# Optimization experiments

Measured on AMD Instinct MI355X. Metric: run time of the kernel, lower is better.

## Reference

```python
import jax, jax.numpy as jnp
import numpy as np

D = 1024; H = 8; QLR = 384; KVLR = 256; NOPE = 128; ROPE = 64; VD = 128
E = 8; TOPK = 2; INTER = 512; NSH = 2; B = 2; T = 2048
QKD = NOPE + ROPE  # 192


def _rms(x, w, eps=1e-6):
    return x * jax.lax.rsqrt(jnp.mean(x * x, axis=-1, keepdims=True) + eps) * w


def _rope(x, cos, sin):
    # x: [B,T,h,ROPE]; pairs are consecutive elements (torch view(...,-1,2)).
    x0 = x[..., 0::2]
    x1 = x[..., 1::2]
    c = cos[None, :, None, :]
    s = sin[None, :, None, :]
    y0 = x0 * c - x1 * s
    y1 = x0 * s + x1 * c
    return jnp.stack([y0, y1], axis=-1).reshape(x.shape)


def setup_inputs() -> dict:
    key = jax.random.key(0)
    ks = jax.random.split(key, 12)
    def w(k, shape, scale=0.02):
        return jax.random.normal(k, shape, dtype=jnp.float32) * scale
    inv = 1.0 / (10000.0 ** (jnp.arange(0, ROPE, 2, dtype=jnp.float32) / ROPE))
    ang = jnp.arange(T, dtype=jnp.float32)[:, None] * inv[None, :]  # [T, ROPE//2]
    return {
        "x": jax.random.normal(ks[0], (B, T, D), dtype=jnp.float32),
        "freqs_cos": jnp.cos(ang),
        "freqs_sin": jnp.sin(ang),
        "rmsn1_w": jnp.ones((D,), jnp.float32),
        "rmsn2_w": jnp.ones((D,), jnp.float32),
        "latent_w": w(ks[1], (D, QLR + KVLR + ROPE)),
        "q_norm_w": jnp.ones((QLR,), jnp.float32),
        "q_up_w": w(ks[2], (QLR, H * QKD)),
        "kv_norm_w": jnp.ones((KVLR,), jnp.float32),
        "kv_up_w": w(ks[3], (KVLR, H * (NOPE + VD))),
        "c_proj_w": w(ks[4], (D, D)),
        "gate_w": w(ks[5], (D, E)),
        "sh_w1": w(ks[6], (D, INTER * NSH)),
        "sh_w2": w(ks[7], (INTER * NSH, D)),
        "sh_w3": w(ks[8], (D, INTER * NSH)),
        "e_w1": w(ks[9], (E, D, INTER)),
        "e_w2": w(ks[10], (E, INTER, D)),
        "e_w3": w(ks[11], (E, D, INTER)),
    }


def reference(x, freqs_cos, freqs_sin, rmsn1_w, rmsn2_w, latent_w, q_norm_w,
              q_up_w, kv_norm_w, kv_up_w, c_proj_w, gate_w, sh_w1, sh_w2,
              sh_w3, e_w1, e_w2, e_w3):
    Bx, Tx, _ = x.shape
    # ---- MLA attention ----
    h = _rms(x, rmsn1_w)
    lat = h @ latent_w
    q_l, kv_l, k_r = jnp.split(lat, [QLR, QLR + KVLR], axis=-1)
    q = (_rms(q_l, q_norm_w) @ q_up_w).reshape(Bx, Tx, H, QKD)
    q_n, q_r = q[..., :NOPE], q[..., NOPE:]
    q_r = _rope(q_r, freqs_cos, freqs_sin)
    q = jnp.concatenate([q_n, q_r], axis=-1)  # [B,T,H,QKD]
    kv = (_rms(kv_l, kv_norm_w) @ kv_up_w).reshape(Bx, Tx, H, NOPE + VD)
    k_n, v = kv[..., :NOPE], kv[..., NOPE:]
    k_r = _rope(k_r[:, :, None, :], freqs_cos, freqs_sin)
    k_r = jnp.broadcast_to(k_r, (Bx, Tx, H, ROPE))
    k = jnp.concatenate([k_n, k_r], axis=-1)
    scale = 1.0 / jnp.sqrt(jnp.float32(QKD))
    scores = jnp.einsum('bqhd,bkhd->bhqk', q, k) * scale
    causal = jnp.tril(jnp.ones((Tx, Tx), dtype=bool))
    scores = jnp.where(causal, scores, jnp.finfo(scores.dtype).min)
    attn = jax.nn.softmax(scores, axis=-1)
    y = jnp.einsum('bhqk,bkhd->bqhd', attn, v).reshape(Bx, Tx, D)
    x = x + y @ c_proj_w
    # ---- DeepSeekMoE ----
    h2 = _rms(x, rmsn2_w).reshape(-1, D)  # [N, D]
    y_sh = (jax.nn.silu(h2 @ sh_w1) * (h2 @ sh_w3)) @ sh_w2
    scores_g = jax.nn.softmax(h2 @ gate_w, axis=-1)  # [N, E]
    w_top, idx = jax.lax.top_k(scores_g, TOPK)  # weights == gathered original scores
    # combine weights per expert (route_scale = 1.0)
    cw = jnp.sum(jax.nn.one_hot(idx, E, dtype=h2.dtype) * w_top[..., None], axis=1)  # [N, E]
    h1 = jnp.einsum('nd,edi->eni', h2, e_w1)
    h3 = jnp.einsum('nd,edi->eni', h2, e_w3)
    out_e = jnp.einsum('eni,eid->end', jax.nn.silu(h1) * h3, e_w2)  # [E, N, D]
    y_moe = y_sh + jnp.einsum('end,ne->nd', out_e, cw)
    return x + y_moe.reshape(Bx, Tx, D)
```

## Files before the change

### kernel.cpp

```cpp
#include <hip/hip_runtime.h>
#include <hip/hip_bf16.h>
#include <math.h>

#define D_ 1024
#define H_ 8
#define QLR_ 384
#define KVLR_ 256
#define NOPE_ 128
#define ROPE_ 64
#define VD_ 128
#define E_ 8
#define INTER_ 512
#define B_ 2
#define T_ 2048
#define QKD_ 192
#define NTOK (B_*T_)
#define LSTR 4608
#define MAXMB 72

typedef __attribute__((ext_vector_type(8))) short short8;
typedef __attribute__((ext_vector_type(4))) float f32x4;
typedef __attribute__((ext_vector_type(4))) unsigned short us4;

__device__ __forceinline__ unsigned short f2bf(float f) {
  union { float f; unsigned u; } v; v.f = f;
  return (unsigned short)((v.u + 0x7FFFu + ((v.u >> 16) & 1u)) >> 16);
}
__device__ __forceinline__ float bf2f(unsigned short h) {
  union { unsigned u; float f; } v; v.u = ((unsigned)h) << 16;
  return v.f;
}

#define GLD16(SRC, DST) __builtin_amdgcn_global_load_lds( \
    (__attribute__((address_space(1))) void*)(SRC), \
    (__attribute__((address_space(3))) void*)(DST), 16, 0, 0)

#define DPPF(v, ctrl) __int_as_float(__builtin_amdgcn_update_dpp(0, __float_as_int(v), ctrl, 0xF, 0xF, true))
__device__ __forceinline__ float dppmax16(float v) {
  v = fmaxf(v, DPPF(v, 0xB1));
  v = fmaxf(v, DPPF(v, 0x4E));
  v = fmaxf(v, DPPF(v, 0x124));
  v = fmaxf(v, DPPF(v, 0x128));
  return v;
}
__device__ __forceinline__ float dppsum16(float v) {
  v += DPPF(v, 0xB1);
  v += DPPF(v, 0x4E);
  v += DPPF(v, 0x124);
  v += DPPF(v, 0x128);
  return v;
}

__global__ __launch_bounds__(256) void transpose_f32_bf16(
    const float* __restrict__ in, unsigned short* __restrict__ out,
    int R, int C, size_t inBS, size_t outBS) {
  __shared__ float tile[32][33];
  const float* inp = in + (size_t)blockIdx.z * inBS;
  unsigned short* outp = out + (size_t)blockIdx.z * outBS;
  int c0 = blockIdx.x * 32, r0 = blockIdx.y * 32;
  int tx = threadIdx.x & 31, ty = threadIdx.x >> 5;
  #pragma unroll
  for (int i = 0; i < 4; ++i) {
    int rr = ty + i * 8;
    tile[rr][tx] = inp[(size_t)(r0 + rr) * C + c0 + tx];
  }
  __syncthreads();
  #pragma unroll
  for (int i = 0; i < 4; ++i) {
    int rr = ty + i * 8;
    outp[(size_t)(c0 + rr) * R + r0 + tx] = f2bf(tile[tx][rr]);
  }
}

__global__ __launch_bounds__(256) void transpose_pair(
    const float* __restrict__ in1, const float* __restrict__ in3,
    unsigned short* __restrict__ out, int K, int C1, size_t inBS, size_t outBS) {
  __shared__ float tile[32][33];
  int z = blockIdx.z; int bat = z >> 1; int f = (z & 1) * 16;
  const float* src = ((z & 1) ? in3 : in1) + (size_t)bat * inBS;
  unsigned short* o = out + (size_t)bat * outBS;
  int c0 = blockIdx.x * 32, r0 = blockIdx.y * 32;
  int tx = threadIdx.x & 31, ty = threadIdx.x >> 5;
  #pragma unroll
  for (int i = 0; i < 4; ++i) {
    int rr = ty + i * 8;
    tile[rr][tx] = src[(size_t)(r0 + rr) * C1 + c0 + tx];
  }
  __syncthreads();
  #pragma unroll
  for (int i = 0; i < 4; ++i) {
    int cc = ty + i * 8;
    int c = c0 + cc;
    int n = ((c >> 4) << 5) + (c & 15) + f;
    o[(size_t)n * K + r0 + tx] = f2bf(tile[tx][cc]);
  }
}

template<typename TI>
__global__ __launch_bounds__(256) void rms_to_bf16(
    const TI* __restrict__ src, int stride, int off, const float* __restrict__ w,
    unsigned short* __restrict__ out, int Dd, int outStride) {
  int row = blockIdx.x;
  const TI* xr = src + (size_t)row * stride + off;
  float ss = 0.f;
  for (int i = threadIdx.x; i < Dd; i += 256) {
    float v;
    if constexpr (sizeof(TI) == 2) v = bf2f((unsigned short)xr[i]); else v = (float)xr[i];
    ss += v * v;
  }
  for (int o = 1; o < 64; o <<= 1) ss += __shfl_xor(ss, o);
  __shared__ float red[4];
  if ((threadIdx.x & 63) == 0) red[threadIdx.x >> 6] = ss;
  __syncthreads();
  float tot = red[0] + red[1] + red[2] + red[3];
  float inv = 1.f / sqrtf(tot / Dd + 1e-6f);
  for (int i = threadIdx.x; i < Dd; i += 256) {
    float v;
    if constexpr (sizeof(TI) == 2) v = bf2f((unsigned short)xr[i]); else v = (float)xr[i];
    out[(size_t)row * outStride + i] = f2bf(v * inv * w[i]);
  }
}

__global__ __launch_bounds__(256) void lat_post(
    const unsigned short* __restrict__ lat, const float* __restrict__ qw,
    const float* __restrict__ kw, const float* __restrict__ fc, const float* __restrict__ fs,
    unsigned short* __restrict__ qn, unsigned short* __restrict__ kvn,
    unsigned short* __restrict__ kr) {
  int row = blockIdx.x, tid = threadIdx.x;
  int lane = tid & 63, wv = tid >> 6;
  const unsigned short* lr = lat + (size_t)row * 768;
  float s1 = 0.f, s2 = 0.f;
  for (int i = tid; i < QLR_; i += 256) { float v = bf2f(lr[i]); s1 += v * v; }
  { float v = bf2f(lr[QLR_ + tid]); s2 = v * v; }
  for (int o = 1; o < 64; o <<= 1) { s1 += __shfl_xor(s1, o); s2 += __shfl_xor(s2, o); }
  __shared__ float red[8];
  if (lane == 0) { red[wv] = s1; red[4 + wv] = s2; }
  __syncthreads();
  float inv1 = 1.f / sqrtf((red[0] + red[1] + red[2] + red[3]) / QLR_ + 1e-6f);
  float inv2 = 1.f / sqrtf((red[4] + red[5] + red[6] + red[7]) / KVLR_ + 1e-6f);
  for (int i = tid; i < QLR_; i += 256)
    qn[(size_t)row * QLR_ + i] = f2bf(bf2f(lr[i]) * inv1 * qw[i]);
  kvn[(size_t)row * KVLR_ + tid] = f2bf(bf2f(lr[QLR_ + tid]) * inv2 * kw[tid]);
  if (tid < 32) {
    int t = row & (T_ - 1);
    float c = fc[t * 32 + tid], s = fs[t * 32 + tid];
    float x0 = bf2f(lr[640 + 2 * tid]), x1 = bf2f(lr[640 + 2 * tid + 1]);
    kr[(size_t)row * ROPE_ + 2 * tid]     = f2bf(x0 * c - x1 * s);
    kr[(size_t)row * ROPE_ + 2 * tid + 1] = f2bf(x0 * s + x1 * c);
  }
}

template<int MODE>
__global__ __launch_bounds__(256) void gemm_bf16(
    const unsigned short* __restrict__ A, const unsigned short* __restrict__ Bt,
    void* __restrict__ Cv, int M, int N, int K,
    const float* __restrict__ addv, unsigned short* __restrict__ vtg) {
  __shared__ __align__(16) unsigned short As[128 * 32];
  __shared__ __align__(16) unsigned short Bs[128 * 32];
  const int tid = threadIdx.x;
  const int lane = tid & 63, wave = tid >> 6;
  const int wm = wave >> 1, wn = wave & 1;
  const int bm = blockIdx.y * 128, bn = blockIdx.x * 128;
  const int r = lane & 15, g = lane >> 4;

  f32x4 acc[4][4];
  #pragma unroll
  for (int i = 0; i < 4; ++i)
    #pragma unroll
    for (int j = 0; j < 4; ++j) acc[i][j] = (f32x4)0.f;

  const int rl0 = wave * 16 + (lane >> 2);
  const int rl1 = rl0 + 64;
  const int kc = (lane & 3) * 8;
  char* AsB = (char*)As; char* BsB = (char*)Bs;

  for (int k0 = 0; k0 < K; k0 += 32) {
    GLD16(A + (size_t)(bm + rl0) * K + k0 + kc, AsB + wave * 1024);
    GLD16(A + (size_t)(bm + rl1) * K + k0 + kc, AsB + (wave + 4) * 1024);
    GLD16(Bt + (size_t)(bn + rl0) * K + k0 + kc, BsB + wave * 1024);
    GLD16(Bt + (size_t)(bn + rl1) * K + k0 + kc, BsB + (wave + 4) * 1024);
    __syncthreads();
    short8 af[4], bfr[4];
    #pragma unroll
    for (int mi = 0; mi < 4; ++mi)
      af[mi] = *(const short8*)(As + (wm * 64 + mi * 16 + r) * 32 + g * 8);
    #pragma unroll
    for (int nj = 0; nj < 4; ++nj)
      bfr[nj] = *(const short8*)(Bs + (wn * 64 + nj * 16 + r) * 32 + g * 8);
    #pragma unroll
    for (int mi = 0; mi < 4; ++mi)
      #pragma unroll
      for (int nj = 0; nj < 4; ++nj)
        acc[mi][nj] = __builtin_amdgcn_mfma_f32_16x16x32_bf16(af[mi], bfr[nj], acc[mi][nj], 0, 0, 0);
    __syncthreads();
  }

  if (MODE == 5) {
    unsigned short* C = (unsigned short*)Cv;
    const int colbase = bn + wn * 64;
    const int b = bm >> 11;
    const int hh = colbase >> 8;
    if ((colbase & 255) < 128) {
      #pragma unroll
      for (int mi = 0; mi < 4; ++mi)
        #pragma unroll
        for (int reg = 0; reg < 4; ++reg) {
          int mrow = bm + wm * 64 + mi * 16 + g * 4 + reg;
          size_t bas = (size_t)mrow * N + colbase + r;
          #pragma unroll
          for (int nj = 0; nj < 4; ++nj) C[bas + nj * 16] = f2bf(acc[mi][nj][reg]);
        }
    } else {
      const int tl0 = (bm & 2047) + wm * 64 + g * 4;
      const int d0 = (colbase & 255) - 128 + r;
      const size_t bhbase = (size_t)(b * 8 + hh) * 64;
      #pragma unroll
      for (int mi = 0; mi < 4; ++mi) {
        int t = tl0 + mi * 16;
        size_t tb = (bhbase + (t >> 5)) * 4096 + (t & 31);
        #pragma unroll
        for (int nj = 0; nj < 4; ++nj) {
          int d = d0 + nj * 16;
          us4 pk;
          #pragma unroll
          for (int reg = 0; reg < 4; ++reg) pk[reg] = f2bf(acc[mi][nj][reg]);
          *(us4*)(vtg + tb + (size_t)d * 32) = pk;
        }
      }
    }
    return;
  }

  const int orow0 = wm * 64 + g * 4;
  const int ocol0 = bn + wn * 64 + r;
  #pragma unroll
  for (int mi = 0; mi < 4; ++mi) {
    #pragma unroll
    for (int reg = 0; reg < 4; ++reg) {
      int mrow = bm + orow0 + mi * 16 + reg;
      if (MODE == 4) {
        unsigned short* C = (unsigned short*)Cv;
        size_t bas2 = (size_t)mrow * (N >> 1) + ((bn + wn * 64) >> 1) + r;
        #pragma unroll
        for (int p = 0; p < 2; ++p) {
          float a = acc[mi][2 * p][reg], b3 = acc[mi][2 * p + 1][reg];
          C[bas2 + p * 16] = f2bf((a / (1.f + __expf(-a))) * b3);
        }
      } else {
        size_t bas = (size_t)mrow * N + ocol0;
        if (MODE == 0) {
          unsigned short* C = (unsigned short*)Cv;
          #pragma unroll
          for (int nj = 0; nj < 4; ++nj) C[bas + nj * 16] = f2bf(acc[mi][nj][reg]);
        } else if (MODE == 1) {
          float* C = (float*)Cv;
          #pragma unroll
          for (int nj = 0; nj < 4; ++nj) C[bas + nj * 16] = acc[mi][nj][reg] + addv[bas + nj * 16];
        } else {
          float* C = (float*)Cv;
          #pragma unroll
          for (int nj = 0; nj < 4; ++nj) C[bas + nj * 16] += acc[mi][nj][reg];
        }
      }
    }
  }
}

__global__ __launch_bounds__(256) void gemm_moe13(
    const unsigned short* __restrict__ A, const unsigned short* __restrict__ W,
    unsigned short* __restrict__ Cb,
    const int* __restrict__ lists, const int* __restrict__ map, const int* __restrict__ sbase) {
  int mb = map[blockIdx.y];
  if (mb < 0) return;
  const int e = mb >> 16, ib = mb & 0xFFFF;
  __shared__ __align__(16) unsigned short As[128 * 32];
  __shared__ __align__(16) unsigned short Bs[128 * 32];
  const int tid = threadIdx.x, lane = tid & 63, wave = tid >> 6;
  const int wm = wave >> 1, wn = wave & 1;
  const int bn = blockIdx.x * 128;
  const int r = lane & 15, g = lane >> 4;

  f32x4 acc[4][4];
  #pragma unroll
  for (int i = 0; i < 4; ++i)
    #pragma unroll
    for (int j = 0; j < 4; ++j) acc[i][j] = (f32x4)0.f;

  const int rl0 = wave * 16 + (lane >> 2), rl1 = rl0 + 64;
  const int kc = (lane & 3) * 8;
  int t0 = lists[e * LSTR + ib * 128 + rl0]; if (t0 < 0) t0 = 0;
  int t1 = lists[e * LSTR + ib * 128 + rl1]; if (t1 < 0) t1 = 0;
  const unsigned short* Wb = W + (size_t)e * 1024 * 1024;
  char* AsB = (char*)As; char* BsB = (char*)Bs;

  for (int k0 = 0; k0 < 1024; k0 += 32) {
    GLD16(A + (size_t)t0 * 1024 + k0 + kc, AsB + wave * 1024);
    GLD16(A + (size_t)t1 * 1024 + k0 + kc, AsB + (wave + 4) * 1024);
    GLD16(Wb + (size_t)(bn + rl0) * 1024 + k0 + kc, BsB + wave * 1024);
    GLD16(Wb + (size_t)(bn + rl1) * 1024 + k0 + kc, BsB + (wave + 4) * 1024);
    __syncthreads();
    short8 af[4], bfr[4];
    #pragma unroll
    for (int mi = 0; mi < 4; ++mi)
      af[mi] = *(const short8*)(As + (wm * 64 + mi * 16 + r) * 32 + g * 8);
    #pragma unroll
    for (int nj = 0; nj < 4; ++nj)
      bfr[nj] = *(const short8*)(Bs + (wn * 64 + nj * 16 + r) * 32 + g * 8);
    #pragma unroll
    for (int mi = 0; mi < 4; ++mi)
      #pragma unroll
      for (int nj = 0; nj < 4; ++nj)
        acc[mi][nj] = __builtin_amdgcn_mfma_f32_16x16x32_bf16(af[mi], bfr[nj], acc[mi][nj], 0, 0, 0);
    __syncthreads();
  }
  const int sb = sbase[e] + ib * 128;
  const int hc = ((bn + wn * 64) >> 1) + r;
  #pragma unroll
  for (int mi = 0; mi < 4; ++mi)
    #pragma unroll
    for (int reg = 0; reg < 4; ++reg) {
      int srow = sb + wm * 64 + mi * 16 + g * 4 + reg;
      #pragma unroll
      for (int p = 0; p < 2; ++p) {
        float a = acc[mi][2 * p][reg], b3 = acc[mi][2 * p + 1][reg];
        Cb[(size_t)srow * 512 + hc + p * 16] = f2bf((a / (1.f + __expf(-a))) * b3);
      }
    }
}

__global__ __launch_bounds__(256) void gemm_moe2(
    const unsigned short* __restrict__ Am, const unsigned short* __restrict__ W,
    float* __restrict__ out,
    const int* __restrict__ lists, const int* __restrict__ map, const int* __restrict__ sbase,
    const float* __restrict__ cw) {
  int mb = map[blockIdx.y];
  if (mb < 0) return;
  const int e = mb >> 16, ib = mb & 0xFFFF;
  __shared__ __align__(16) unsigned short As[128 * 32];
  __shared__ __align__(16) unsigned short Bs[128 * 32];
  const int tid = threadIdx.x, lane = tid & 63, wave = tid >> 6;
  const int wm = wave >> 1, wn = wave & 1;
  const int bn = blockIdx.x * 128;
  const int r = lane & 15, g = lane >> 4;

  f32x4 acc[4][4];
  #pragma unroll
  for (int i = 0; i < 4; ++i)
    #pragma unroll
    for (int j = 0; j < 4; ++j) acc[i][j] = (f32x4)0.f;

  const int rl0 = wave * 16 + (lane >> 2), rl1 = rl0 + 64;
  const int kc = (lane & 3) * 8;
  const int sb = sbase[e] + ib * 128;
  const unsigned short* Wb = W + (size_t)e * 512 * 1024;
  char* AsB = (char*)As; char* BsB = (char*)Bs;

  for (int k0 = 0; k0 < 512; k0 += 32) {
    GLD16(Am + (size_t)(sb + rl0) * 512 + k0 + kc, AsB + wave * 1024);
    GLD16(Am + (size_t)(sb + rl1) * 512 + k0 + kc, AsB + (wave + 4) * 1024);
    GLD16(Wb + (size_t)(bn + rl0) * 512 + k0 + kc, BsB + wave * 1024);
    GLD16(Wb + (size_t)(bn + rl1) * 512 + k0 + kc, BsB + (wave + 4) * 1024);
    __syncthreads();
    short8 af[4], bfr[4];
    #pragma unroll
    for (int mi = 0; mi < 4; ++mi)
      af[mi] = *(const short8*)(As + (wm * 64 + mi * 16 + r) * 32 + g * 8);
    #pragma unroll
    for (int nj = 0; nj < 4; ++nj)
      bfr[nj] = *(const short8*)(Bs + (wn * 64 + nj * 16 + r) * 32 + g * 8);
    #pragma unroll
    for (int mi = 0; mi < 4; ++mi)
      #pragma unroll
      for (int nj = 0; nj < 4; ++nj)
        acc[mi][nj] = __builtin_amdgcn_mfma_f32_16x16x32_bf16(af[mi], bfr[nj], acc[mi][nj], 0, 0, 0);
    __syncthreads();
  }
  const int ocol0 = bn + wn * 64 + r;
  #pragma unroll
  for (int mi = 0; mi < 4; ++mi)
    #pragma unroll
    for (int reg = 0; reg < 4; ++reg) {
      int orow = wm * 64 + mi * 16 + g * 4 + reg;
      int tok = lists[e * LSTR + ib * 128 + orow];
      if (tok >= 0) {
        float wt = cw[(size_t)tok * E_ + e];
        #pragma unroll
        for (int nj = 0; nj < 4; ++nj)
          atomicAdd(out + (size_t)tok * 1024 + ocol0 + nj * 16, acc[mi][nj][reg] * wt);
      }
    }
}

#define AQ 64
#define AK 32
#define VP 40
__global__ __launch_bounds__(256) void attn_mfma(
    const unsigned short* __restrict__ q,
    const unsigned short* __restrict__ kv,
    const unsigned short* __restrict__ kr,
    const unsigned short* __restrict__ vt,
    const float* __restrict__ fcos, const float* __restrict__ fsin,
    unsigned short* __restrict__ po,
    float* __restrict__ pml) {
  __shared__ __align__(16) unsigned short Ks[AK * 192];
  __shared__ __align__(16) unsigned short Vl[128 * VP];
  __shared__ __align__(16) unsigned short Ps[4 * 16 * VP];
  const int tid = threadIdx.x, lane = tid & 63, wave = tid >> 6;
  const int r = lane & 15, g = lane >> 4;
  const int bh = blockIdx.y, b = bh >> 3, h = bh & 7;
  const int qt = gridDim.x - 1 - blockIdx.x;
  const int q0 = qt * AQ;
  const int half = blockIdx.z;
  const int hnt = qt + 1;
  const int kb = half * hnt, ke = kb + hnt;
  const size_t bT = (size_t)b * T_;
  const unsigned short* vbase = vt + (size_t)bh * 64 * 4096;
  char* KsB = (char*)Ks;

  short8 qf[6];
  const int qrow = q0 + wave * 16 + r;
  {
    const unsigned short* qb = q + ((bT + qrow) * H_ + h) * 192;
    #pragma unroll
    for (int kk = 0; kk < 6; ++kk) qf[kk] = *(const short8*)(qb + kk * 32 + g * 8);
    #pragma unroll
    for (int kk = 4; kk < 6; ++kk) {
      int i0 = (kk - 4) * 16 + g * 4;
      #pragma unroll
      for (int p = 0; p < 4; ++p) {
        float cc = fcos[qrow * 32 + i0 + p], sn = fsin[qrow * 32 + i0 + p];
        float x0 = bf2f((unsigned short)qf[kk][2 * p]), x1 = bf2f((unsigned short)qf[kk][2 * p + 1]);
        qf[kk][2 * p]     = (short)f2bf(x0 * cc - x1 * sn);
        qf[kk][2 * p + 1] = (short)f2bf(x0 * sn + x1 * cc);
      }
    }
  }

  float m_i[4], l_i[4];
  f32x4 o[8];
  #pragma unroll
  for (int i = 0; i < 4; ++i) { m_i[i] = -1e30f; l_i[i] = 0.f; }
  #pragma unroll
  for (int cb = 0; cb < 8; ++cb) o[cb] = (f32x4)0.f;

  const float scale2 = 0.07216878364870322f * 1.44269504088896f;

  short8 kreg[3], vreg[2];
  int krow[3], kcol[3];
  #pragma unroll
  for (int it = 0; it < 3; ++it) {
    int c = tid + it * 256;
    krow[it] = c / 24; kcol[it] = c % 24;
    kreg[it] = (kcol[it] < 16)
      ? *(const short8*)(kv + ((bT + kb * AK + krow[it]) * H_ + h) * 256 + kcol[it] * 8)
      : *(const short8*)(kr + (bT + kb * AK + krow[it]) * 64 + (kcol[it] - 16) * 8);
  }
  #pragma unroll
  for (int it = 0; it < 2; ++it) {
    int x = tid + it * 256;
    vreg[it] = *(const short8*)(vbase + (size_t)kb * 4096 + x * 8);
  }

  for (int kt = kb; kt < ke; ++kt) {
    __builtin_amdgcn_s_barrier();
    __builtin_amdgcn_sched_barrier(0);
    #pragma unroll
    for (int it = 0; it < 3; ++it)
      *(short8*)(KsB + ((krow[it] * 384 + kcol[it] * 16) ^ ((krow[it] & 7) << 4))) = kreg[it];
    #pragma unroll
    for (int it = 0; it < 2; ++it) {
      int x = tid + it * 256;
      *(short8*)(Vl + (x >> 2) * VP + (x & 3) * 8) = vreg[it];
    }
    asm volatile("s_waitcnt lgkmcnt(0)" ::: "memory");
    __builtin_amdgcn_s_barrier();
    __builtin_amdgcn_sched_barrier(0);

    if (kt + 1 < ke) {
      int k1 = (kt + 1) * AK;
      #pragma unroll
      for (int it = 0; it < 3; ++it)
        kreg[it] = (kcol[it] < 16)
          ? *(const short8*)(kv + ((bT + k1 + krow[it]) * H_ + h) * 256 + kcol[it] * 8)
          : *(const short8*)(kr + (bT + k1 + krow[it]) * 64 + (kcol[it] - 16) * 8);
      #pragma unroll
      for (int it = 0; it < 2; ++it) {
        int x = tid + it * 256;
        vreg[it] = *(const short8*)(vbase + (size_t)(kt + 1) * 4096 + x * 8);
      }
    }

    const int k0 = kt * AK;
    f32x4 sf0 = (f32x4)0.f, sf1 = (f32x4)0.f;
    {
      int ksw = (r & 7) << 4;
      __builtin_amdgcn_s_setprio(1);
      #pragma unroll
      for (int kk = 0; kk < 6; ++kk) {
        short8 b0 = *(const short8*)(KsB + ((r * 384 + kk * 64 + g * 16) ^ ksw));
        short8 b1 = *(const short8*)(KsB + (((16 + r) * 384 + kk * 64 + g * 16) ^ ksw));
        sf0 = __builtin_amdgcn_mfma_f32_16x16x32_bf16(qf[kk], b0, sf0, 0, 0, 0);
        sf1 = __builtin_amdgcn_mfma_f32_16x16x32_bf16(qf[kk], b1, sf1, 0, 0, 0);
      }
      __builtin_amdgcn_s_setprio(0);
    }

    float fac[4];
    bool needs = false;
    const bool bnd = (k0 + AK > q0);
    #pragma unroll
    for (int reg = 0; reg < 4; ++reg) {
      float s0 = sf0[reg] * scale2;
      float s1 = sf1[reg] * scale2;
      if (bnd) {
        int qp = q0 + wave * 16 + g * 4 + reg;
        if (k0 + r > qp) s0 = -1e30f;
        if (k0 + 16 + r > qp) s1 = -1e30f;
      }
      float mt = dppmax16(fmaxf(s0, s1));
      float fc = 1.f, mn = m_i[reg];
      if (mt > mn + 8.f) {
        mn = mt; fc = exp2f(m_i[reg] - mn); m_i[reg] = mn; needs = true;
      }
      float e0 = exp2f(s0 - mn), e1 = exp2f(s1 - mn);
      float rs = dppsum16(e0 + e1);
      l_i[reg] = l_i[reg] * fc + rs;
      fac[reg] = fc;
      __hip_bfloat162 pk = __float22bfloat162_rn(float2{e0, e1});
      unsigned u = *(unsigned*)&pk;
      int prow = g * 4 + reg;
      Ps[wave * 16 * VP + prow * VP + r] = (unsigned short)u;
      Ps[wave * 16 * VP + prow * VP + 16 + r] = (unsigned short)(u >> 16);
    }
    if (__any(needs)) {
      #pragma unroll
      for (int cb = 0; cb < 8; ++cb)
        #pragma unroll
        for (int reg = 0; reg < 4; ++reg) o[cb][reg] *= fac[reg];
    }
    short8 pa = *(const short8*)(Ps + wave * 16 * VP + r * VP + g * 8);
    __builtin_amdgcn_s_setprio(1);
    #pragma unroll
    for (int cb = 0; cb < 8; ++cb) {
      short8 vb = *(const short8*)(Vl + (cb * 16 + r) * VP + g * 8);
      o[cb] = __builtin_amdgcn_mfma_f32_16x16x32_bf16(pa, vb, o[cb], 0, 0, 0);
    }
    __builtin_amdgcn_s_setprio(0);
  }

  const int slab = (bh * 32 + qt) * 2 + half;
  unsigned short* pob = po + (size_t)slab * 8192;
  float* pmlb = pml + (size_t)slab * 128;
  #pragma unroll
  for (int reg = 0; reg < 4; ++reg) {
    int row = wave * 16 + g * 4 + reg;
    if (r == 0) { pmlb[row * 2] = m_i[reg]; pmlb[row * 2 + 1] = l_i[reg]; }
    #pragma unroll
    for (int cb = 0; cb < 8; ++cb)
      pob[row * 128 + cb * 16 + r] = f2bf(o[cb][reg]);
  }
}

__global__ __launch_bounds__(256) void attn_combine(
    const unsigned short* __restrict__ po, const float* __restrict__ pml,
    unsigned short* __restrict__ y) {
  const int qt = blockIdx.x, bh = blockIdx.y, b = bh >> 3, h = bh & 7;
  const int s0 = (bh * 32 + qt) * 2, s1 = s0 + 1;
  const int row = threadIdx.x >> 2;
  const int qp = threadIdx.x & 3;
  float m0 = pml[(size_t)s0 * 128 + row * 2], l0 = pml[(size_t)s0 * 128 + row * 2 + 1];
  float m1 = pml[(size_t)s1 * 128 + row * 2], l1 = pml[(size_t)s1 * 128 + row * 2 + 1];
  float m = fmaxf(m0, m1);
  float e0 = exp2f(m0 - m), e1 = exp2f(m1 - m);
  float inv = 1.f / (l0 * e0 + l1 * e1);
  e0 *= inv; e1 *= inv;
  const unsigned short* o0 = po + (size_t)s0 * 8192 + row * 128 + qp * 32;
  const unsigned short* o1 = po + (size_t)s1 * 8192 + row * 128 + qp * 32;
  unsigned short* yb = y + ((size_t)(b * T_ + qt * 64 + row)) * 1024 + h * 128 + qp * 32;
  #pragma unroll
  for (int v = 0; v < 4; ++v) {
    short8 a = *(const short8*)(o0 + v * 8);
    short8 c = *(const short8*)(o1 + v * 8);
    short8 w;
    #pragma unroll
    for (int j = 0; j < 8; ++j)
      w[j] = (short)f2bf(bf2f((unsigned short)a[j]) * e0 + bf2f((unsigned short)c[j]) * e1);
    *(short8*)(yb + v * 8) = w;
  }
}

__global__ __launch_bounds__(256) void rms2_gate(
    const float* __restrict__ xo, const float* __restrict__ rw, const float* __restrict__ gw,
    unsigned short* __restrict__ h2b, float* __restrict__ cw) {
  int row = blockIdx.x, tid = threadIdx.x;
  int lane = tid & 63, wv = tid >> 6;
  const float* xr = xo + (size_t)row * D_;
  float v[4]; float ss = 0.f;
  #pragma unroll
  for (int j = 0; j < 4; ++j) { v[j] = xr[tid + j * 256]; ss += v[j] * v[j]; }
  for (int o = 1; o < 64; o <<= 1) ss += __shfl_xor(ss, o);
  __shared__ float red[4];
  if (lane == 0) red[wv] = ss;
  __syncthreads();
  float inv = 1.f / sqrtf((red[0] + red[1] + red[2] + red[3]) / D_ + 1e-6f);
  float a[E_] = {0, 0, 0, 0, 0, 0, 0, 0};
  #pragma unroll
  for (int j = 0; j < 4; ++j) {
    int i = tid + j * 256;
    float hv = v[j] * inv * rw[i];
    h2b[(size_t)row * D_ + i] = f2bf(hv);
    const float* wr = gw + (size_t)i * E_;
    #pragma unroll
    for (int e = 0; e < E_; ++e) a[e] += hv * wr[e];
  }
  #pragma unroll
  for (int e = 0; e < E_; ++e) {
    float t = a[e];
    for (int o = 1; o < 64; o <<= 1) t += __shfl_xor(t, o);
    a[e] = t;
  }
  __shared__ float ga[4][E_];
  if (lane == 0)
    #pragma unroll
    for (int e = 0; e < E_; ++e) ga[wv][e] = a[e];
  __syncthreads();
  if (tid == 0) {
    float lg[E_];
    #pragma unroll
    for (int e = 0; e < E_; ++e) lg[e] = ga[0][e] + ga[1][e] + ga[2][e] + ga[3][e];
    float mx = lg[0];
    #pragma unroll
    for (int e = 1; e < E_; ++e) mx = fmaxf(mx, lg[e]);
    float sum = 0.f; float p[E_];
    #pragma unroll
    for (int e = 0; e < E_; ++e) { p[e] = __expf(lg[e] - mx); sum += p[e]; }
    float is = 1.f / sum;
    int i1 = 0; float b1 = p[0];
    #pragma unroll
    for (int e = 1; e < E_; ++e) if (p[e] > b1) { b1 = p[e]; i1 = e; }
    int i2 = -1; float b2 = -1.f;
    #pragma unroll
    for (int e = 0; e < E_; ++e) if (e != i1 && p[e] > b2) { b2 = p[e]; i2 = e; }
    #pragma unroll
    for (int e = 0; e < E_; ++e)
      cw[(size_t)row * E_ + e] = (e == i1) ? b1 * is : (e == i2 ? b2 * is : 0.f);
  }
}

__global__ __launch_bounds__(256) void moe_build(const float* __restrict__ cw,
                                                 int* __restrict__ lists, int* __restrict__ counts) {
  int e = blockIdx.x, tid = threadIdx.x;
  int lane = tid & 63, wv = tid >> 6;
  __shared__ int wsum[4];
  __shared__ int base;
  if (tid == 0) base = 0;
  __syncthreads();
  for (int c0 = 0; c0 < NTOK; c0 += 256) {
    int tok = c0 + tid;
    bool f = cw[(size_t)tok * E_ + e] > 0.f;
    unsigned long long m = __ballot(f);
    int pos = __popcll(m & ((1ull << lane) - 1ull));
    if (lane == 0) wsum[wv] = __popcll(m);
    __syncthreads();
    int woff = base;
    #pragma unroll
    for (int w = 0; w < 4; ++w) if (w < wv) woff += wsum[w];
    if (f) lists[e * LSTR + woff + pos] = tok;
    __syncthreads();
    if (tid == 0) base += wsum[0] + wsum[1] + wsum[2] + wsum[3];
    __syncthreads();
  }
  int cnt = base;
  int padded = (cnt + 127) & ~127;
  for (int i2 = cnt + tid; i2 < padded; i2 += 256) lists[e * LSTR + i2] = -1;
  if (tid == 0) { counts[e] = cnt; counts[8 + e] = padded >> 7; }
}

__global__ void moe_finalize(const int* __restrict__ counts, int* __restrict__ map,
                             int* __restrict__ sbase) {
  if (threadIdx.x == 0 && blockIdx.x == 0) {
    int cum = 0;
    for (int e = 0; e < E_; ++e) {
      sbase[e] = cum * 128;
      int nb = counts[8 + e];
      for (int i = 0; i < nb; ++i) map[cum + i] = (e << 16) | i;
      cum += nb;
    }
    for (; cum < MAXMB; ++cum) map[cum] = -1;
  }
}

extern "C" void kernel_launch(void* const* d_in, const int* in_sizes, int n_in,
                              void* d_out, int out_size, void* d_ws, size_t ws_size,
                              hipStream_t stream) {
  const float* x        = (const float*)d_in[0];
  const float* fcos     = (const float*)d_in[1];
  const float* fsin     = (const float*)d_in[2];
  const float* rmsn1_w  = (const float*)d_in[3];
  const float* rmsn2_w  = (const float*)d_in[4];
  const float* latent_w = (const float*)d_in[5];
  const float* q_norm_w = (const float*)d_in[6];
  const float* q_up_w   = (const float*)d_in[7];
  const float* kv_norm_w= (const float*)d_in[8];
  const float* kv_up_w  = (const float*)d_in[9];
  const float* c_proj_w = (const float*)d_in[10];
  const float* gate_w   = (const float*)d_in[11];
  const float* sh_w1    = (const float*)d_in[12];
  const float* sh_w2    = (const float*)d_in[13];
  const float* sh_w3    = (const float*)d_in[14];
  const float* e_w1     = (const float*)d_in[15];
  const float* e_w2     = (const float*)d_in[16];
  const float* e_w3     = (const float*)d_in[17];
  float* out = (float*)d_out;

  char* base = (char*)d_ws;
  size_t off = 0;
  auto take = [&](size_t bytes) { char* p = base + off; off += (bytes + 255) & ~(size_t)255; return p; };
  unsigned short* Wlat  = (unsigned short*)take((size_t)768 * 1024 * 2);
  unsigned short* Wqup  = (unsigned short*)take((size_t)1536 * 384 * 2);
  unsigned short* Wkv   = (unsigned short*)take((size_t)2048 * 256 * 2);
  unsigned short* Wcp   = (unsigned short*)take((size_t)1024 * 1024 * 2);
  unsigned short* Wsh13 = (unsigned short*)take((size_t)2048 * 1024 * 2);
  unsigned short* Wsh2  = (unsigned short*)take((size_t)1024 * 1024 * 2);
  unsigned short* Wew13 = (unsigned short*)take((size_t)8 * 1024 * 1024 * 2);
  unsigned short* Wew2  = (unsigned short*)take((size_t)8 * 1024 * 512 * 2);
  float* cw             = (float*)take((size_t)NTOK * E_ * 4);
  int* lists            = (int*)take((size_t)E_ * LSTR * 4);
  int* counts           = (int*)take(64 * 4);
  int* map              = (int*)take(MAXMB * 4);
  int* sbase            = (int*)take(E_ * 4);
  unsigned short* Vtg   = (unsigned short*)take((size_t)16 * 64 * 4096 * 2);
  unsigned short* kr    = (unsigned short*)take((size_t)NTOK * 64 * 2);
  float* pml            = (float*)take((size_t)1024 * 128 * 4);

  size_t actStart = off;
  size_t aoff = actStart;
  auto takeA = [&](size_t bytes) { char* p = base + aoff; aoff += (bytes + 255) & ~(size_t)255; return p; };
  unsigned short* h_bf = (unsigned short*)takeA((size_t)NTOK * 1024 * 2);
  unsigned short* lat  = (unsigned short*)takeA((size_t)NTOK * 768 * 2);
  unsigned short* qn   = (unsigned short*)takeA((size_t)NTOK * 384 * 2);
  unsigned short* kvn  = (unsigned short*)takeA((size_t)NTOK * 256 * 2);
  unsigned short* qq   = (unsigned short*)takeA((size_t)NTOK * 1536 * 2);
  unsigned short* kvb  = (unsigned short*)takeA((size_t)NTOK * 2048 * 2);
  unsigned short* y    = (unsigned short*)takeA((size_t)NTOK * 1024 * 2);

  unsigned short* po   = (unsigned short*)(base + actStart);

  size_t coff = actStart;
  auto takeC = [&](size_t bytes) { char* p = base + coff; coff += (bytes + 255) & ~(size_t)255; return p; };
  unsigned short* h2b  = (unsigned short*)takeC((size_t)NTOK * 1024 * 2);
  unsigned short* t1m  = (unsigned short*)takeC((size_t)NTOK * 1024 * 2);
  unsigned short* ehm  = (unsigned short*)takeC((size_t)9216 * 512 * 2);

  dim3 blk(256);

  transpose_f32_bf16<<<dim3(22, 32, 1), blk, 0, stream>>>(latent_w, Wlat, 1024, 704, 0, 0);
  transpose_f32_bf16<<<dim3(48, 12, 1), blk, 0, stream>>>(q_up_w, Wqup, 384, 1536, 0, 0);
  transpose_f32_bf16<<<dim3(64, 8, 1), blk, 0, stream>>>(kv_up_w, Wkv, 256, 2048, 0, 0);
  transpose_f32_bf16<<<dim3(32, 32, 1), blk, 0, stream>>>(c_proj_w, Wcp, 1024, 1024, 0, 0);
  transpose_f32_bf16<<<dim3(32, 32, 1), blk, 0, stream>>>(sh_w2, Wsh2, 1024, 1024, 0, 0);
  transpose_pair<<<dim3(32, 32, 2), blk, 0, stream>>>(sh_w1, sh_w3, Wsh13, 1024, 1024, 0, 0);
  transpose_pair<<<dim3(16, 32, 16), blk, 0, stream>>>(e_w1, e_w3, Wew13, 1024, 512,
      (size_t)1024 * 512, (size_t)1024 * 1024);
  transpose_f32_bf16<<<dim3(32, 16, 8), blk, 0, stream>>>(e_w2, Wew2, 512, 1024,
      (size_t)512 * 1024, (size_t)1024 * 512);

  rms_to_bf16<float><<<NTOK, blk, 0, stream>>>(x, D_, 0, rmsn1_w, h_bf, D_, D_);
  gemm_bf16<0><<<dim3(6, 32), blk, 0, stream>>>(h_bf, Wlat, lat, NTOK, 768, 1024, nullptr, nullptr);
  lat_post<<<NTOK, blk, 0, stream>>>(lat, q_norm_w, kv_norm_w, fcos, fsin, qn, kvn, kr);
  gemm_bf16<0><<<dim3(12, 32), blk, 0, stream>>>(qn, Wqup, qq, NTOK, 1536, 384, nullptr, nullptr);
  gemm_bf16<5><<<dim3(16, 32), blk, 0, stream>>>(kvn, Wkv, kvb, NTOK, 2048, 256, nullptr, Vtg);
  attn_mfma<<<dim3(T_ / AQ, B_ * H_, 2), blk, 0, stream>>>(qq, kvb, kr, Vtg, fcos, fsin, po, pml);
  attn_combine<<<dim3(T_ / AQ, B_ * H_), blk, 0, stream>>>(po, pml, y);
  gemm_bf16<1><<<dim3(8, 32), blk, 0, stream>>>(y, Wcp, out, NTOK, 1024, 1024, x, nullptr);
  rms2_gate<<<NTOK, blk, 0, stream>>>(out, rmsn2_w, gate_w, h2b, cw);
  moe_build<<<E_, blk, 0, stream>>>(cw, lists, counts);
  moe_finalize<<<1, 64, 0, stream>>>(counts, map, sbase);
  gemm_bf16<4><<<dim3(16, 32), blk, 0, stream>>>(h2b, Wsh13, t1m, NTOK, 2048, 1024, nullptr, nullptr);
  gemm_bf16<2><<<dim3(8, 32), blk, 0, stream>>>(t1m, Wsh2, out, NTOK, 1024, 1024, nullptr, nullptr);
  gemm_moe13<<<dim3(8, MAXMB), blk, 0, stream>>>(h2b, Wew13, ehm, lists, map, sbase);
  gemm_moe2<<<dim3(8, MAXMB), blk, 0, stream>>>(ehm, Wew2, out, lists, map, sbase, cw);
}
```

Measured before the change: 415.1 us.

## Merge q/kv up-projections and shared/routed FFN GEMMs into combined launches

Combines the q-up and kv-up projection GEMMs into one grid with branch-selected operands, and merges the shared-expert and routed-expert FFN GEMMs into single launches for the w1/w3 stage and the w2 stage. The aim is fewer kernel launches and better GPU fill, since the small routed-expert grids can run alongside the shared-expert tiles instead of waiting for them. In exchange, the shared w2 output now goes through atomicAdd instead of a plain read-modify-write, and the mixed-K branches add some divergence in block setup.

```diff
diff --git a/kernel.cpp b/kernel.cpp
--- a/kernel.cpp
+++ b/kernel.cpp
@@ -154,7 +154,7 @@
 __global__ __launch_bounds__(256) void gemm_bf16(
     const unsigned short* __restrict__ A, const unsigned short* __restrict__ Bt,
     void* __restrict__ Cv, int M, int N, int K,
-    const float* __restrict__ addv, unsigned short* __restrict__ vtg) {
+    const float* __restrict__ addv) {
   __shared__ __align__(16) unsigned short As[128 * 32];
   __shared__ __align__(16) unsigned short Bs[128 * 32];
   const int tid = threadIdx.x;
@@ -195,8 +195,91 @@
     __syncthreads();
   }
 
-  if (MODE == 5) {
-    unsigned short* C = (unsigned short*)Cv;
+  const int orow0 = wm * 64 + g * 4;
+  const int ocol0 = bn + wn * 64 + r;
+  #pragma unroll
+  for (int mi = 0; mi < 4; ++mi) {
+    #pragma unroll
+    for (int reg = 0; reg < 4; ++reg) {
+      int mrow = bm + orow0 + mi * 16 + reg;
+      size_t bas = (size_t)mrow * N + ocol0;
+      if (MODE == 0) {
+        unsigned short* C = (unsigned short*)Cv;
+        #pragma unroll
+        for (int nj = 0; nj < 4; ++nj) C[bas + nj * 16] = f2bf(acc[mi][nj][reg]);
+      } else {
+        float* C = (float*)Cv;
+        #pragma unroll
+        for (int nj = 0; nj < 4; ++nj) C[bas + nj * 16] = acc[mi][nj][reg] + addv[bas + nj * 16];
+      }
+    }
+  }
+}
+
+__global__ __launch_bounds__(256) void gemm_qkv(
+    const unsigned short* __restrict__ qn, const unsigned short* __restrict__ Wqup,
+    const unsigned short* __restrict__ kvn, const unsigned short* __restrict__ Wkv,
+    unsigned short* __restrict__ qq, unsigned short* __restrict__ kvb,
+    unsigned short* __restrict__ vtg) {
+  __shared__ __align__(16) unsigned short As[128 * 32];
+  __shared__ __align__(16) unsigned short Bs[128 * 32];
+  const int tid = threadIdx.x;
+  const int lane = tid & 63, wave = tid >> 6;
+  const int wm = wave >> 1, wn = wave & 1;
+  const bool isQ = blockIdx.x < 12;
+  const int bx = isQ ? blockIdx.x : blockIdx.x - 12;
+  const unsigned short* A  = isQ ? qn : kvn;
+  const unsigned short* Bt = isQ ? Wqup : Wkv;
+  const int N = isQ ? 1536 : 2048;
+  const int K = isQ ? QLR_ : KVLR_;
+  const int bm = blockIdx.y * 128, bn = bx * 128;
+  const int r = lane & 15, g = lane >> 4;
+
+  f32x4 acc[4][4];
+  #pragma unroll
+  for (int i = 0; i < 4; ++i)
+    #pragma unroll
+    for (int j = 0; j < 4; ++j) acc[i][j] = (f32x4)0.f;
+
+  const int rl0 = wave * 16 + (lane >> 2);
+  const int rl1 = rl0 + 64;
+  const int kc = (lane & 3) * 8;
+  char* AsB = (char*)As; char* BsB = (char*)Bs;
+
+  for (int k0 = 0; k0 < K; k0 += 32) {
+    GLD16(A + (size_t)(bm + rl0) * K + k0 + kc, AsB + wave * 1024);
+    GLD16(A + (size_t)(bm + rl1) * K + k0 + kc, AsB + (wave + 4) * 1024);
+    GLD16(Bt + (size_t)(bn + rl0) * K + k0 + kc, BsB + wave * 1024);
+    GLD16(Bt + (size_t)(bn + rl1) * K + k0 + kc, BsB + (wave + 4) * 1024);
+    __syncthreads();
+    short8 af[4], bfr[4];
+    #pragma unroll
+    for (int mi = 0; mi < 4; ++mi)
+      af[mi] = *(const short8*)(As + (wm * 64 + mi * 16 + r) * 32 + g * 8);
+    #pragma unroll
+    for (int nj = 0; nj < 4; ++nj)
+      bfr[nj] = *(const short8*)(Bs + (wn * 64 + nj * 16 + r) * 32 + g * 8);
+    #pragma unroll
+    for (int mi = 0; mi < 4; ++mi)
+      #pragma unroll
+      for (int nj = 0; nj < 4; ++nj)
+        acc[mi][nj] = __builtin_amdgcn_mfma_f32_16x16x32_bf16(af[mi], bfr[nj], acc[mi][nj], 0, 0, 0);
+    __syncthreads();
+  }
+
+  if (isQ) {
+    const int orow0 = wm * 64 + g * 4;
+    const int ocol0 = bn + wn * 64 + r;
+    #pragma unroll
+    for (int mi = 0; mi < 4; ++mi)
+      #pragma unroll
+      for (int reg = 0; reg < 4; ++reg) {
+        int mrow = bm + orow0 + mi * 16 + reg;
+        size_t bas = (size_t)mrow * 1536 + ocol0;
+        #pragma unroll
+        for (int nj = 0; nj < 4; ++nj) qq[bas + nj * 16] = f2bf(acc[mi][nj][reg]);
+      }
+  } else {
     const int colbase = bn + wn * 64;
     const int b = bm >> 11;
     const int hh = colbase >> 8;
@@ -206,9 +289,9 @@
         #pragma unroll
         for (int reg = 0; reg < 4; ++reg) {
           int mrow = bm + wm * 64 + mi * 16 + g * 4 + reg;
-          size_t bas = (size_t)mrow * N + colbase + r;
+          size_t bas = (size_t)mrow * 2048 + colbase + r;
           #pragma unroll
-          for (int nj = 0; nj < 4; ++nj) C[bas + nj * 16] = f2bf(acc[mi][nj][reg]);
+          for (int nj = 0; nj < 4; ++nj) kvb[bas + nj * 16] = f2bf(acc[mi][nj][reg]);
         }
     } else {
       const int tl0 = (bm & 2047) + wm * 64 + g * 4;
@@ -228,138 +311,146 @@
         }
       }
     }
-    return;
-  }
-
-  const int orow0 = wm * 64 + g * 4;
-  const int ocol0 = bn + wn * 64 + r;
-  #pragma unroll
-  for (int mi = 0; mi < 4; ++mi) {
-    #pragma unroll
-    for (int reg = 0; reg < 4; ++reg) {
-      int mrow = bm + orow0 + mi * 16 + reg;
-      if (MODE == 4) {
-        unsigned short* C = (unsigned short*)Cv;
-        size_t bas2 = (size_t)mrow * (N >> 1) + ((bn + wn * 64) >> 1) + r;
+  }
+}
+
+__global__ __launch_bounds__(256) void gemm_ffn13(
+    const unsigned short* __restrict__ h2b, const unsigned short* __restrict__ Wsh13,
+    unsigned short* __restrict__ t1m,
+    const unsigned short* __restrict__ Wew13, unsigned short* __restrict__ ehm,
+    const int* __restrict__ lists, const int* __restrict__ map, const int* __restrict__ sbase) {
+  __shared__ __align__(16) unsigned short As[128 * 32];
+  __shared__ __align__(16) unsigned short Bs[128 * 32];
+  const int i = blockIdx.x;
+  const bool isSh = i < 512;
+  const int tid = threadIdx.x, lane = tid & 63, wave = tid >> 6;
+  const int wm = wave >> 1, wn = wave & 1;
+  const int r = lane & 15, g = lane >> 4;
+  const int rl0 = wave * 16 + (lane >> 2), rl1 = rl0 + 64;
+  const int kc = (lane & 3) * 8;
+
+  int bn, e = 0, ib = 0, bm = 0;
+  const unsigned short* Bt;
+  int ar0, ar1;
+  const unsigned short* A;
+  if (isSh) {
+    bn = (i & 15) * 128; bm = (i >> 4) * 128;
+    Bt = Wsh13; A = h2b;
+    ar0 = bm + rl0; ar1 = bm + rl1;
+  } else {
+    int j = i - 512;
+    bn = (j & 7) * 128;
+    int mb = map[j >> 3];
+    if (mb < 0) return;
+    e = mb >> 16; ib = mb & 0xFFFF;
+    Bt = Wew13 + (size_t)e * 1024 * 1024; A = h2b;
+    ar0 = lists[e * LSTR + ib * 128 + rl0]; if (ar0 < 0) ar0 = 0;
+    ar1 = lists[e * LSTR + ib * 128 + rl1]; if (ar1 < 0) ar1 = 0;
+  }
+
+  f32x4 acc[4][4];
+  #pragma unroll
+  for (int a = 0; a < 4; ++a)
+    #pragma unroll
+    for (int bj = 0; bj < 4; ++bj) acc[a][bj] = (f32x4)0.f;
+  char* AsB = (char*)As; char* BsB = (char*)Bs;
+
+  for (int k0 = 0; k0 < 1024; k0 += 32) {
+    GLD16(A + (size_t)ar0 * 1024 + k0 + kc, AsB + wave * 1024);
+    GLD16(A + (size_t)ar1 * 1024 + k0 + kc, AsB + (wave + 4) * 1024);
+    GLD16(Bt + (size_t)(bn + rl0) * 1024 + k0 + kc, BsB + wave * 1024);
+    GLD16(Bt + (size_t)(bn + rl1) * 1024 + k0 + kc, BsB + (wave + 4) * 1024);
+    __syncthreads();
+    short8 af[4], bfr[4];
+    #pragma unroll
+    for (int mi = 0; mi < 4; ++mi)
+      af[mi] = *(const short8*)(As + (wm * 64 + mi * 16 + r) * 32 + g * 8);
+    #pragma unroll
+    for (int nj = 0; nj < 4; ++nj)
+      bfr[nj] = *(const short8*)(Bs + (wn * 64 + nj * 16 + r) * 32 + g * 8);
+    #pragma unroll
+    for (int mi = 0; mi < 4; ++mi)
+      #pragma unroll
+      for (int nj = 0; nj < 4; ++nj)
+        acc[mi][nj] = __builtin_amdgcn_mfma_f32_16x16x32_bf16(af[mi], bfr[nj], acc[mi][nj], 0, 0, 0);
+    __syncthreads();
+  }
+
+  if (isSh) {
+    const int hc = ((bn + wn * 64) >> 1) + r;
+    #pragma unroll
+    for (int mi = 0; mi < 4; ++mi)
+      #pragma unroll
+      for (int reg = 0; reg < 4; ++reg) {
+        int mrow = bm + wm * 64 + mi * 16 + g * 4 + reg;
         #pragma unroll
         for (int p = 0; p < 2; ++p) {
           float a = acc[mi][2 * p][reg], b3 = acc[mi][2 * p + 1][reg];
-          C[bas2 + p * 16] = f2bf((a / (1.f + __expf(-a))) * b3);
+          t1m[(size_t)mrow * 1024 + hc + p * 16] = f2bf((a / (1.f + __expf(-a))) * b3);
         }
-      } else {
-        size_t bas = (size_t)mrow * N + ocol0;
-        if (MODE == 0) {
-          unsigned short* C = (unsigned short*)Cv;
-          #pragma unroll
-          for (int nj = 0; nj < 4; ++nj) C[bas + nj * 16] = f2bf(acc[mi][nj][reg]);
-        } else if (MODE == 1) {
-          float* C = (float*)Cv;
-          #pragma unroll
-          for (int nj = 0; nj < 4; ++nj) C[bas + nj * 16] = acc[mi][nj][reg] + addv[bas + nj * 16];
-        } else {
-          float* C = (float*)Cv;
-          #pragma unroll
-          for (int nj = 0; nj < 4; ++nj) C[bas + nj * 16] += acc[mi][nj][reg];
+      }
+  } else {
+    const int sb = sbase[e] + ib * 128;
+    const int hc = ((bn + wn * 64) >> 1) + r;
+    #pragma unroll
+    for (int mi = 0; mi < 4; ++mi)
+      #pragma unroll
+      for (int reg = 0; reg < 4; ++reg) {
+        int srow = sb + wm * 64 + mi * 16 + g * 4 + reg;
+        #pragma unroll
+        for (int p = 0; p < 2; ++p) {
+          float a = acc[mi][2 * p][reg], b3 = acc[mi][2 * p + 1][reg];
+          ehm[(size_t)srow * 512 + hc + p * 16] = f2bf((a / (1.f + __expf(-a))) * b3);
         }
       }
-    }
-  }
-}
-
-__global__ __launch_bounds__(256) void gemm_moe13(
-    const unsigned short* __restrict__ A, const unsigned short* __restrict__ W,
-    unsigned short* __restrict__ Cb,
-    const int* __restrict__ lists, const int* __restrict__ map, const int* __restrict__ sbase) {
-  int mb = map[blockIdx.y];
-  if (mb < 0) return;
-  const int e = mb >> 16, ib = mb & 0xFFFF;
-  __shared__ __align__(16) unsigned short As[128 * 32];
-  __shared__ __align__(16) unsigned short Bs[128 * 32];
-  const int tid = threadIdx.x, lane = tid & 63, wave = tid >> 6;
-  const int wm = wave >> 1, wn = wave & 1;
-  const int bn = blockIdx.x * 128;
-  const int r = lane & 15, g = lane >> 4;
-
-  f32x4 acc[4][4];
-  #pragma unroll
-  for (int i = 0; i < 4; ++i)
-    #pragma unroll
-    for (int j = 0; j < 4; ++j) acc[i][j] = (f32x4)0.f;
-
-  const int rl0 = wave * 16 + (lane >> 2), rl1 = rl0 + 64;
-  const int kc = (lane & 3) * 8;
-  int t0 = lists[e * LSTR + ib * 128 + rl0]; if (t0 < 0) t0 = 0;
-  int t1 = lists[e * LSTR + ib * 128 + rl1]; if (t1 < 0) t1 = 0;
-  const unsigned short* Wb = W + (size_t)e * 1024 * 1024;
-  char* AsB = (char*)As; char* BsB = (char*)Bs;
-
-  for (int k0 = 0; k0 < 1024; k0 += 32) {
-    GLD16(A + (size_t)t0 * 1024 + k0 + kc, AsB + wave * 1024);
-    GLD16(A + (size_t)t1 * 1024 + k0 + kc, AsB + (wave + 4) * 1024);
-    GLD16(Wb + (size_t)(bn + rl0) * 1024 + k0 + kc, BsB + wave * 1024);
-    GLD16(Wb + (size_t)(bn + rl1) * 1024 + k0 + kc, BsB + (wave + 4) * 1024);
-    __syncthreads();
-    short8 af[4], bfr[4];
-    #pragma unroll
-    for (int mi = 0; mi < 4; ++mi)
-      af[mi] = *(const short8*)(As + (wm * 64 + mi * 16 + r) * 32 + g * 8);
-    #pragma unroll
-    for (int nj = 0; nj < 4; ++nj)
-      bfr[nj] = *(const short8*)(Bs + (wn * 64 + nj * 16 + r) * 32 + g * 8);
-    #pragma unroll
-    for (int mi = 0; mi < 4; ++mi)
-      #pragma unroll
-      for (int nj = 0; nj < 4; ++nj)
-        acc[mi][nj] = __builtin_amdgcn_mfma_f32_16x16x32_bf16(af[mi], bfr[nj], acc[mi][nj], 0, 0, 0);
-    __syncthreads();
-  }
-  const int sb = sbase[e] + ib * 128;
-  const int hc = ((bn + wn * 64) >> 1) + r;
-  #pragma unroll
-  for (int mi = 0; mi < 4; ++mi)
-    #pragma unroll
-    for (int reg = 0; reg < 4; ++reg) {
-      int srow = sb + wm * 64 + mi * 16 + g * 4 + reg;
-      #pragma unroll
-      for (int p = 0; p < 2; ++p) {
-        float a = acc[mi][2 * p][reg], b3 = acc[mi][2 * p + 1][reg];
-        Cb[(size_t)srow * 512 + hc + p * 16] = f2bf((a / (1.f + __expf(-a))) * b3);
-      }
-    }
-}
-
-__global__ __launch_bounds__(256) void gemm_moe2(
-    const unsigned short* __restrict__ Am, const unsigned short* __restrict__ W,
+  }
+}
+
+__global__ __launch_bounds__(256) void gemm_ffn2(
+    const unsigned short* __restrict__ t1m, const unsigned short* __restrict__ Wsh2,
+    const unsigned short* __restrict__ ehm, const unsigned short* __restrict__ Wew2,
     float* __restrict__ out,
     const int* __restrict__ lists, const int* __restrict__ map, const int* __restrict__ sbase,
     const float* __restrict__ cw) {
-  int mb = map[blockIdx.y];
-  if (mb < 0) return;
-  const int e = mb >> 16, ib = mb & 0xFFFF;
   __shared__ __align__(16) unsigned short As[128 * 32];
   __shared__ __align__(16) unsigned short Bs[128 * 32];
+  const int i = blockIdx.x;
+  const bool isSh = i < 256;
   const int tid = threadIdx.x, lane = tid & 63, wave = tid >> 6;
   const int wm = wave >> 1, wn = wave & 1;
-  const int bn = blockIdx.x * 128;
   const int r = lane & 15, g = lane >> 4;
-
-  f32x4 acc[4][4];
-  #pragma unroll
-  for (int i = 0; i < 4; ++i)
-    #pragma unroll
-    for (int j = 0; j < 4; ++j) acc[i][j] = (f32x4)0.f;
-
   const int rl0 = wave * 16 + (lane >> 2), rl1 = rl0 + 64;
   const int kc = (lane & 3) * 8;
-  const int sb = sbase[e] + ib * 128;
-  const unsigned short* Wb = W + (size_t)e * 512 * 1024;
+
+  int bn, e = 0, ib = 0, bm = 0, K, sb = 0;
+  const unsigned short* A;
+  const unsigned short* Bt;
+  if (isSh) {
+    bn = (i & 7) * 128; bm = (i >> 3) * 128;
+    A = t1m; Bt = Wsh2; K = 1024;
+  } else {
+    int j = i - 256;
+    bn = (j & 7) * 128;
+    int mb = map[j >> 3];
+    if (mb < 0) return;
+    e = mb >> 16; ib = mb & 0xFFFF;
+    sb = sbase[e] + ib * 128;
+    A = ehm; Bt = Wew2 + (size_t)e * 512 * 1024; K = 512;
+    bm = sb;
+  }
+
+  f32x4 acc[4][4];
+  #pragma unroll
+  for (int a = 0; a < 4; ++a)
+    #pragma unroll
+    for (int bj = 0; bj < 4; ++bj) acc[a][bj] = (f32x4)0.f;
   char* AsB = (char*)As; char* BsB = (char*)Bs;
 
-  for (int k0 = 0; k0 < 512; k0 += 32) {
-    GLD16(Am + (size_t)(sb + rl0) * 512 + k0 + kc, AsB + wave * 1024);
-    GLD16(Am + (size_t)(sb + rl1) * 512 + k0 + kc, AsB + (wave + 4) * 1024);
-    GLD16(Wb + (size_t)(bn + rl0) * 512 + k0 + kc, BsB + wave * 1024);
-    GLD16(Wb + (size_t)(bn + rl1) * 512 + k0 + kc, BsB + (wave + 4) * 1024);
+  for (int k0 = 0; k0 < K; k0 += 32) {
+    GLD16(A + (size_t)(bm + rl0) * K + k0 + kc, AsB + wave * 1024);
+    GLD16(A + (size_t)(bm + rl1) * K + k0 + kc, AsB + (wave + 4) * 1024);
+    GLD16(Bt + (size_t)(bn + rl0) * K + k0 + kc, BsB + wave * 1024);
+    GLD16(Bt + (size_t)(bn + rl1) * K + k0 + kc, BsB + (wave + 4) * 1024);
     __syncthreads();
     short8 af[4], bfr[4];
     #pragma unroll
@@ -375,20 +466,33 @@
         acc[mi][nj] = __builtin_amdgcn_mfma_f32_16x16x32_bf16(af[mi], bfr[nj], acc[mi][nj], 0, 0, 0);
     __syncthreads();
   }
+
   const int ocol0 = bn + wn * 64 + r;
-  #pragma unroll
-  for (int mi = 0; mi < 4; ++mi)
-    #pragma unroll
-    for (int reg = 0; reg < 4; ++reg) {
-      int orow = wm * 64 + mi * 16 + g * 4 + reg;
-      int tok = lists[e * LSTR + ib * 128 + orow];
-      if (tok >= 0) {
-        float wt = cw[(size_t)tok * E_ + e];
+  if (isSh) {
+    #pragma unroll
+    for (int mi = 0; mi < 4; ++mi)
+      #pragma unroll
+      for (int reg = 0; reg < 4; ++reg) {
+        int mrow = bm + wm * 64 + mi * 16 + g * 4 + reg;
         #pragma unroll
         for (int nj = 0; nj < 4; ++nj)
-          atomicAdd(out + (size_t)tok * 1024 + ocol0 + nj * 16, acc[mi][nj][reg] * wt);
-      }
-    }
+          atomicAdd(out + (size_t)mrow * 1024 + ocol0 + nj * 16, acc[mi][nj][reg]);
+      }
+  } else {
+    #pragma unroll
+    for (int mi = 0; mi < 4; ++mi)
+      #pragma unroll
+      for (int reg = 0; reg < 4; ++reg) {
+        int orow = wm * 64 + mi * 16 + g * 4 + reg;
+        int tok = lists[e * LSTR + ib * 128 + orow];
+        if (tok >= 0) {
+          float wt = cw[(size_t)tok * E_ + e];
+          #pragma unroll
+          for (int nj = 0; nj < 4; ++nj)
+            atomicAdd(out + (size_t)tok * 1024 + ocol0 + nj * 16, acc[mi][nj][reg] * wt);
+        }
+      }
+  }
 }
 
 #define AQ 64
@@ -766,18 +870,15 @@
       (size_t)512 * 1024, (size_t)1024 * 512);
 
   rms_to_bf16<float><<<NTOK, blk, 0, stream>>>(x, D_, 0, rmsn1_w, h_bf, D_, D_);
-  gemm_bf16<0><<<dim3(6, 32), blk, 0, stream>>>(h_bf, Wlat, lat, NTOK, 768, 1024, nullptr, nullptr);
+  gemm_bf16<0><<<dim3(6, 32), blk, 0, stream>>>(h_bf, Wlat, lat, NTOK, 768, 1024, nullptr);
   lat_post<<<NTOK, blk, 0, stream>>>(lat, q_norm_w, kv_norm_w, fcos, fsin, qn, kvn, kr);
-  gemm_bf16<0><<<dim3(12, 32), blk, 0, stream>>>(qn, Wqup, qq, NTOK, 1536, 384, nullptr, nullptr);
-  gemm_bf16<5><<<dim3(16, 32), blk, 0, stream>>>(kvn, Wkv, kvb, NTOK, 2048, 256, nullptr, Vtg);
+  gemm_qkv<<<dim3(28, 32), blk, 0, stream>>>(qn, Wqup, kvn, Wkv, qq, kvb, Vtg);
   attn_mfma<<<dim3(T_ / AQ, B_ * H_, 2), blk, 0, stream>>>(qq, kvb, kr, Vtg, fcos, fsin, po, pml);
   attn_combine<<<dim3(T_ / AQ, B_ * H_), blk, 0, stream>>>(po, pml, y);
-  gemm_bf16<1><<<dim3(8, 32), blk, 0, stream>>>(y, Wcp, out, NTOK, 1024, 1024, x, nullptr);
+  gemm_bf16<1><<<dim3(8, 32), blk, 0, stream>>>(y, Wcp, out, NTOK, 1024, 1024, x);
   rms2_gate<<<NTOK, blk, 0, stream>>>(out, rmsn2_w, gate_w, h2b, cw);
   moe_build<<<E_, blk, 0, stream>>>(cw, lists, counts);
   moe_finalize<<<1, 64, 0, stream>>>(counts, map, sbase);
-  gemm_bf16<4><<<dim3(16, 32), blk, 0, stream>>>(h2b, Wsh13, t1m, NTOK, 2048, 1024, nullptr, nullptr);
-  gemm_bf16<2><<<dim3(8, 32), blk, 0, stream>>>(t1m, Wsh2, out, NTOK, 1024, 1024, nullptr, nullptr);
-  gemm_moe13<<<dim3(8, MAXMB), blk, 0, stream>>>(h2b, Wew13, ehm, lists, map, sbase);
-  gemm_moe2<<<dim3(8, MAXMB), blk, 0, stream>>>(ehm, Wew2, out, lists, map, sbase, cw);
-}
+  gemm_ffn13<<<dim3(1088), blk, 0, stream>>>(h2b, Wsh13, t1m, Wew13, ehm, lists, map, sbase);
+  gemm_ffn2<<<dim3(832), blk, 0, stream>>>(t1m, Wsh2, ehm, Wew2, out, lists, map, sbase, cw);
+}
```

New measurement: 397.8 us. 4.2% less time.
